# Performance work log

Hardware: AMD Instinct MI355X
Metric: run time of the kernel (lower is better)

Reference implementation:

```python
import jax, jax.numpy as jnp
import numpy as np

E = 1024   # embd_size
H = 16     # heads_num
DH = E // H
DFF = 4 * E
B, T = 2, 2048


def layer_norm(x, g, b, eps=1e-5):
    mu = jnp.mean(x, axis=-1, keepdims=True)
    var = jnp.var(x, axis=-1, keepdims=True)
    return (x - mu) * jax.lax.rsqrt(var + eps) * g + b


def setup_inputs() -> dict:
    key = jax.random.key(0)
    ks = jax.random.split(key, 12)
    s = 0.02
    return {
        "x": jax.random.normal(ks[0], (B, T, E), dtype=jnp.float32),
        "Wq": jax.random.normal(ks[1], (E, E), dtype=jnp.float32) * s,
        "Wk": jax.random.normal(ks[2], (E, E), dtype=jnp.float32) * s,
        "Wv": jax.random.normal(ks[3], (E, E), dtype=jnp.float32) * s,
        "Wo": jax.random.normal(ks[4], (E, E), dtype=jnp.float32) * s,
        "bo": jnp.zeros((E,), dtype=jnp.float32),
        "W1": jax.random.normal(ks[5], (E, DFF), dtype=jnp.float32) * s,
        "b1": jnp.zeros((DFF,), dtype=jnp.float32),
        "W2": jax.random.normal(ks[6], (DFF, E), dtype=jnp.float32) * s,
        "b2": jnp.zeros((E,), dtype=jnp.float32),
        "g1": jnp.ones((E,), dtype=jnp.float32),
        "be1": jnp.zeros((E,), dtype=jnp.float32),
        "g2": jnp.ones((E,), dtype=jnp.float32),
        "be2": jnp.zeros((E,), dtype=jnp.float32),
    }


def reference(x, Wq, Wk, Wv, Wo, bo, W1, b1, W2, b2, g1, be1, g2, be2):
    Bx, Tx, C = x.shape
    # --- self-attention sublayer ---
    h = layer_norm(x, g1, be1)
    # per-head projections; heads concatenated along output dim == stacked weights
    q = (h @ Wq).reshape(Bx, Tx, H, DH)  # [B,T,H,Dh]
    k = (h @ Wk).reshape(Bx, Tx, H, DH)
    v = (h @ Wv).reshape(Bx, Tx, H, DH)
    # NOTE: original scales by full embd_size**-0.5 (C = x.shape[-1]), not head_size
    scale = C ** (-0.5)
    scores = jnp.einsum("bqhd,bkhd->bhqk", q, k) * scale  # [B,H,T,T]
    mask = jnp.tril(jnp.ones((Tx, Tx), dtype=bool))
    scores = jnp.where(mask, scores, -jnp.inf)
    attn = jax.nn.softmax(scores, axis=-1)
    o = jnp.einsum("bhqk,bkhd->bqhd", attn, v).reshape(Bx, Tx, C)
    sa = o @ Wo + bo
    x = x + sa
    # --- feed-forward sublayer ---
    h2 = layer_norm(x, g2, be2)
    ff = jax.nn.relu(h2 @ W1 + b1) @ W2 + b2
    return x + ff
```

## Files before the change

### kernel.cpp

```cpp
#include <hip/hip_runtime.h>
#include <hip/hip_bf16.h>
#include <math.h>

#define Bn 2
#define Tn 2048
#define En 1024
#define Hn 16
#define DFFn 4096
#define Mn (Bn*Tn)
#define QKVLD 3072

typedef __hip_bfloat16 bf16;
typedef unsigned short u16;
typedef unsigned int u32;
typedef __attribute__((ext_vector_type(8))) short short8;
typedef __attribute__((ext_vector_type(4))) float f32x4;

typedef __attribute__((address_space(1))) const void cg_void;
typedef __attribute__((address_space(3))) void lds_void;

#define QSC 0.0450842200278f

#define HBAR() asm volatile("s_waitcnt lgkmcnt(0)\n\ts_barrier" ::: "memory")

__device__ __forceinline__ u16 f2bf(float f) {
    bf16 h = __float2bfloat16(f);
    u16 u; __builtin_memcpy(&u, &h, 2); return u;
}
__device__ __forceinline__ float bf2f(u16 u) {
    u32 x = ((u32)u) << 16; float f; __builtin_memcpy(&f, &x, 4); return f;
}

__global__ __launch_bounds__(256)
void transpose_w4(const float* __restrict__ s0, const float* __restrict__ s1,
                  const float* __restrict__ s2, const float* __restrict__ s3,
                  u16* __restrict__ d0, u16* __restrict__ d1,
                  u16* __restrict__ d2, u16* __restrict__ d3) {
    const float* src = (blockIdx.z == 0) ? s0 : (blockIdx.z == 1) ? s1
                     : (blockIdx.z == 2) ? s2 : s3;
    u16* dst = (blockIdx.z == 0) ? d0 : (blockIdx.z == 1) ? d1
             : (blockIdx.z == 2) ? d2 : d3;
    __shared__ float t[64][65];
    const int r0 = blockIdx.y * 64, c0 = blockIdx.x * 64;
    const int tr = threadIdx.x >> 6, tc = threadIdx.x & 63;
#pragma unroll
    for (int i = 0; i < 16; i++)
        t[tr + i * 4][tc] = src[(size_t)(r0 + tr + i * 4) * 1024 + c0 + tc];
    __syncthreads();
#pragma unroll
    for (int i = 0; i < 16; i++)
        dst[(size_t)(c0 + tr + i * 4) * 1024 + r0 + tc] = f2bf(t[tc][tr + i * 4]);
}

__global__ __launch_bounds__(256)
void transpose_w(const float* __restrict__ src, u16* __restrict__ dst,
                 int R, int C) {
    __shared__ float t[64][65];
    const int r0 = blockIdx.y * 64, c0 = blockIdx.x * 64;
    const int tr = threadIdx.x >> 6, tc = threadIdx.x & 63;
#pragma unroll
    for (int i = 0; i < 16; i++)
        t[tr + i * 4][tc] = src[(size_t)(r0 + tr + i * 4) * C + c0 + tc];
    __syncthreads();
#pragma unroll
    for (int i = 0; i < 16; i++)
        dst[(size_t)(c0 + tr + i * 4) * R + r0 + tc] = f2bf(t[tc][tr + i * 4]);
}

__global__ __launch_bounds__(256)
void vcopy_t(const u16* __restrict__ QKV, u16* __restrict__ Vg) {
    const int bh = blockIdx.z;
    const int t0 = blockIdx.y * 64;
    __shared__ u16 t[64][65];
    const int tr = threadIdx.x >> 6, tc = threadIdx.x & 63;
    const u16* src = QKV + (size_t)(bh >> 4) * 2048 * QKVLD + 2048 + (bh & 15) * 64;
#pragma unroll
    for (int i = 0; i < 16; i++)
        t[tr + i * 4][tc] = src[(size_t)(t0 + tr + i * 4) * QKVLD + tc];
    __syncthreads();
    u16* dst = Vg + (size_t)bh * 64 * 2048;
#pragma unroll
    for (int i = 0; i < 16; i++)
        dst[(size_t)(tr + i * 4) * 2048 + t0 + tc] = t[tc][tr + i * 4];
}

template<typename AT>
__global__ __launch_bounds__(256)
void ln_kernel(const AT* __restrict__ x, const float* __restrict__ g,
               const float* __restrict__ b, u16* __restrict__ out) {
    const int row = blockIdx.x;
    const int tid = threadIdx.x;
    const AT* xp = x + (size_t)row * En;
    float v[4];
    float s = 0.f, sq = 0.f;
#pragma unroll
    for (int i = 0; i < 4; i++) {
        if constexpr (sizeof(AT) == 2) v[i] = bf2f(xp[tid + i * 256]);
        else                           v[i] = (float)xp[tid + i * 256];
        s += v[i];
        sq += v[i] * v[i];
    }
    __shared__ float rs[256], rq[256];
    rs[tid] = s; rq[tid] = sq;
    __syncthreads();
    for (int st = 128; st > 0; st >>= 1) {
        if (tid < st) { rs[tid] += rs[tid + st]; rq[tid] += rq[tid + st]; }
        __syncthreads();
    }
    const float mu  = rs[0] * (1.0f / En);
    const float var = rq[0] * (1.0f / En) - mu * mu;
    const float inv = rsqrtf(var + 1e-5f);
#pragma unroll
    for (int i = 0; i < 4; i++) {
        const int c = tid + i * 256;
        out[(size_t)row * En + c] = f2bf((v[i] - mu) * inv * g[c] + b[c]);
    }
}

__global__ __launch_bounds__(256)
void ff2_init(const u16* __restrict__ X1, const float* __restrict__ b2,
              float* __restrict__ out) {
    const int row = blockIdx.x;
    const int c = threadIdx.x * 4;
    ushort4 a = *(const ushort4*)&X1[(size_t)row * En + c];
    float4 bb = *(const float4*)&b2[c];
    float4 o;
    o.x = bf2f(a.x) + bb.x;
    o.y = bf2f(a.y) + bb.y;
    o.z = bf2f(a.z) + bb.z;
    o.w = bf2f(a.w) + bb.w;
    *(float4*)&out[(size_t)row * En + c] = o;
}

template<int HAS_BIAS, int RELU, int SPLITC>
__global__ __launch_bounds__(512, 2)
void gemm256(const u16* __restrict__ A, int ldA,
             const u16* __restrict__ Wt, int ldW,
             const float* __restrict__ bias,
             u16* __restrict__ Cout, u16* __restrict__ Cout2,
             int ldC, int Kd) {
    __shared__ __align__(16) u16 As[2][256 * 64];
    __shared__ __align__(16) u16 Bs[2][256 * 64];
    const int tid  = threadIdx.x;
    const int lane = tid & 63, wv = tid >> 6;
    const int quad = lane >> 4, l16 = lane & 15;
    const int wr = wv >> 2, wc = wv & 3;
    const int lr8 = lane >> 3;
    const int gcg = (lane & 7) ^ lr8;

    const int m0 = blockIdx.y * 256, n0 = blockIdx.x * 256;

    f32x4 acc[8][4] = {};

    auto stage = [&](int buf, int kt) {
#pragma unroll
        for (int i = 0; i < 4; i++) {
            const int rbase = wv * 32 + i * 8;
            __builtin_amdgcn_global_load_lds(
                (cg_void*)(const void*)&A[(size_t)(m0 + rbase + lr8) * ldA + kt + gcg * 8],
                (lds_void*)(void*)&As[buf][rbase * 64], 16, 0, 0);
        }
#pragma unroll
        for (int i = 0; i < 4; i++) {
            const int rbase = wv * 32 + i * 8;
            __builtin_amdgcn_global_load_lds(
                (cg_void*)(const void*)&Wt[(size_t)(n0 + rbase + lr8) * ldW + kt + gcg * 8],
                (lds_void*)(void*)&Bs[buf][rbase * 64], 16, 0, 0);
        }
    };
    auto compute = [&](int buf) {
        const int swz = l16 & 7;
#pragma unroll
        for (int ks = 0; ks < 2; ks++) {
            short8 a[8], b[4];
#pragma unroll
            for (int mf = 0; mf < 8; mf++)
                a[mf] = *(const short8*)&As[buf][(wr * 128 + mf * 16 + l16) * 64 +
                         (((ks * 4 + quad) ^ swz) * 8)];
#pragma unroll
            for (int nf = 0; nf < 4; nf++)
                b[nf] = *(const short8*)&Bs[buf][(wc * 64 + nf * 16 + l16) * 64 +
                         (((ks * 4 + quad) ^ swz) * 8)];
#pragma unroll
            for (int mf = 0; mf < 8; mf++)
#pragma unroll
                for (int nf = 0; nf < 4; nf++)
                    acc[mf][nf] = __builtin_amdgcn_mfma_f32_16x16x32_bf16(
                        a[mf], b[nf], acc[mf][nf], 0, 0, 0);
        }
    };

    stage(0, 0);
    asm volatile("s_waitcnt vmcnt(0)" ::: "memory");
    __builtin_amdgcn_s_barrier();
    const int NT = Kd >> 6;
    for (int t = 0; t < NT; ++t) {
        const int cur = t & 1;
        if (t + 1 < NT) stage(cur ^ 1, (t + 1) * 64);
        compute(cur);
        asm volatile("s_waitcnt vmcnt(0) lgkmcnt(0)" ::: "memory");
        __builtin_amdgcn_s_barrier();
    }

#pragma unroll
    for (int mf = 0; mf < 8; mf++) {
#pragma unroll
        for (int r = 0; r < 4; r++) {
            const int gm = m0 + wr * 128 + mf * 16 + quad * 4 + r;
#pragma unroll
            for (int nf = 0; nf < 4; nf++) {
                const int gn = n0 + wc * 64 + nf * 16 + l16;
                const int cn = SPLITC ? (gn & 2047) : gn;
                float c = acc[mf][nf][r];
                if (HAS_BIAS) c += bias[gn];
                if (RELU) c = fmaxf(c, 0.f);
                u16* Cp = (SPLITC && gn >= 2048) ? Cout2 : Cout;
                Cp[(size_t)gm * ldC + cn] = f2bf(c);
            }
        }
    }
}

template<int TM, int HAS_BIAS, int RELU, int RES, int OUT_F32, int SCQ,
         int SPLITC, int SPLITA, int ATOM = 0, int XSWZ = 0, int PIPE = 0>
__global__ __launch_bounds__(256)
void gemm_bt(const u16* __restrict__ A, const u16* __restrict__ A2, int ldA,
             const u16* __restrict__ Wt, int ldW,
             const float* __restrict__ bias, const void* __restrict__ res,
             void* __restrict__ Cout, void* __restrict__ Cout2,
             int ldC, int Kd) {
    constexpr int IF = TM / 32;
    constexpr int LD = TM / 64 + 2;
    constexpr int RB = PIPE ? 4 : 1;
    __shared__ __align__(16) u16 As[RB][TM * 32];
    __shared__ __align__(16) u16 Bs[RB][128 * 32];
    const int tid  = threadIdx.x;
    const int lane = tid & 63, wv = tid >> 6;
    const int quad = lane >> 4, l16 = lane & 15;

    int bx = blockIdx.x, by = blockIdx.y, bz = blockIdx.z;
    if (XSWZ) {
        const int GX = gridDim.x, GY = gridDim.y;
        const int L = (bz * GY + by) * GX + bx;
        const int xcd = L & 7, slot = L >> 3;
        const int p = slot / GX;
        bx = slot - p * GX;
        const int yz = p * 8 + xcd;
        by = yz & (GY - 1);
        bz = yz >> __builtin_ctz(GY);
    }

    const int m0 = by * TM, n0 = bx * 128;
    const int rw = (wv >> 1) * (TM / 2), cw = (wv & 1) * 64;
    const int lr  = lane >> 2;
    const int gsw = ((lane & 3) ^ ((lane >> 3) & 3)) * 8;
    const int psw = (quad ^ ((l16 >> 1) & 3)) * 8;

    f32x4 acc[IF][4] = {};

    auto stage = [&](int buf, int kt) {
        const u16* Ap = (SPLITA && kt >= 2048) ? A2 : A;
        const int  kk = SPLITA ? (kt & 2047) : kt;
#pragma unroll
        for (int t = 0; t < TM / 64; t++) {
            const int row = wv * (TM / 4) + t * 16;
            __builtin_amdgcn_global_load_lds(
                (cg_void*)(const void*)&Ap[(size_t)(m0 + row + lr) * ldA + kk + gsw],
                (lds_void*)(void*)&As[buf][row * 32], 16, 0, 0);
        }
#pragma unroll
        for (int t = 0; t < 2; t++) {
            const int row = wv * 32 + t * 16;
            __builtin_amdgcn_global_load_lds(
                (cg_void*)(const void*)&Wt[(size_t)(n0 + row + lr) * ldW + kt + gsw],
                (lds_void*)(void*)&Bs[buf][row * 32], 16, 0, 0);
        }
    };
    auto compute = [&](int buf) {
        short8 af[IF], bfr[4];
#pragma unroll
        for (int i = 0; i < IF; i++)
            af[i] = *(const short8*)&As[buf][(rw + i * 16 + l16) * 32 + psw];
#pragma unroll
        for (int j = 0; j < 4; j++)
            bfr[j] = *(const short8*)&Bs[buf][(cw + j * 16 + l16) * 32 + psw];
#pragma unroll
        for (int i = 0; i < IF; i++)
#pragma unroll
            for (int j = 0; j < 4; j++)
                acc[i][j] = __builtin_amdgcn_mfma_f32_16x16x32_bf16(
                    af[i], bfr[j], acc[i][j], 0, 0, 0);
    };

    const int kbase = ATOM ? bz * Kd : 0;

    if constexpr (PIPE == 0) {
        for (int kt = kbase; kt < kbase + Kd; kt += 32) {
            __syncthreads();
            stage(0, kt);
            __syncthreads();
            compute(0);
        }
    } else {
        const int NI = Kd >> 5;
        stage(0, kbase);
        stage(1, kbase + 32);
        stage(2, kbase + 64);
        int bc = 0, bs = 3;
        for (int it = 0; it < NI; ++it) {
            if (it + 3 < NI) {
                stage(bs, kbase + (it + 3) * 32);
                if (++bs == RB) bs = 0;
            }
            const int rem = (NI - 1 - it) < 3 ? (NI - 1 - it) : 3;
            if (rem == 3) {
                if constexpr (LD == 4) asm volatile("s_waitcnt vmcnt(12)" ::: "memory");
                else                   asm volatile("s_waitcnt vmcnt(9)"  ::: "memory");
            } else if (rem == 2) {
                if constexpr (LD == 4) asm volatile("s_waitcnt vmcnt(8)"  ::: "memory");
                else                   asm volatile("s_waitcnt vmcnt(6)"  ::: "memory");
            } else if (rem == 1) {
                if constexpr (LD == 4) asm volatile("s_waitcnt vmcnt(4)"  ::: "memory");
                else                   asm volatile("s_waitcnt vmcnt(3)"  ::: "memory");
            } else {
                asm volatile("s_waitcnt vmcnt(0)" ::: "memory");
            }
            __builtin_amdgcn_s_barrier();
            compute(bc);
            if (++bc == RB) bc = 0;
            asm volatile("s_waitcnt lgkmcnt(0)" ::: "memory");
            __builtin_amdgcn_s_barrier();
        }
    }

    const float qscale = (SCQ && n0 < 1024) ? QSC : 1.0f;
    void* Cp = (SPLITC && n0 >= 2048) ? Cout2 : Cout;
#pragma unroll
    for (int i = 0; i < IF; i++) {
#pragma unroll
        for (int r = 0; r < 4; r++) {
            const int gm = m0 + rw + i * 16 + quad * 4 + r;
#pragma unroll
            for (int j = 0; j < 4; j++) {
                const int gn = n0 + cw + j * 16 + l16;
                const int cn = SPLITC ? (gn & 2047) : gn;
                float c = acc[i][j][r];
                if (HAS_BIAS) c += bias[gn];
                if (RELU) c = fmaxf(c, 0.f);
                if (RES == 1) c += ((const float*)res)[(size_t)gm * ldC + cn];
                if (RES == 2) c += bf2f(((const u16*)res)[(size_t)gm * ldC + cn]);
                if (SCQ) c *= qscale;
                if (ATOM) {
                    atomicAdd(&((float*)Cp)[(size_t)gm * ldC + cn], c);
                } else if (OUT_F32) {
                    ((float*)Cp)[(size_t)gm * ldC + cn] = c;
                } else {
                    ((u16*)Cp)[(size_t)gm * ldC + cn] = f2bf(c);
                }
            }
        }
    }
}

__global__ __launch_bounds__(256)
void flash_pass1(const u16* __restrict__ QKV, const u16* __restrict__ Vg,
                 u16* __restrict__ Op0, u16* __restrict__ Op1qkv,
                 float* __restrict__ stats) {
    const int pr = blockIdx.x >> 1, half = blockIdx.x & 1;
    const int hh = blockIdx.y, bb = blockIdx.z;
    const int tid  = threadIdx.x;
    const int lane = tid & 63, wv = tid >> 6;
    const int quad = lane >> 4, l16 = lane & 15;

    __shared__ __align__(16) u16 Ks[2][64 * 64];
    __shared__ __align__(16) u16 Vt[2][64 * 64];
    __shared__ __align__(16) u16 Ps[4][16 * 64];

    const size_t rowbase = (size_t)(bb * Tn) * QKVLD;
    const u16* Vgh = Vg + (size_t)(bb * Hn + hh) * 64 * 2048;

    const int sr = tid >> 2;
    const int p0 = (tid & 3) | ((sr & 1) << 2);
    const int p1 = p0 ^ 4;
    const int g0 = p0 ^ (sr & 7), g1 = p1 ^ (sr & 7);
    const int lsw = l16 & 7;

    uint4 kA, kB, vA, vB;
    auto prefetch = [&](int kt) {
        const size_t kb = rowbase + (size_t)(kt * 64 + sr) * QKVLD + 1024 + hh * 64;
        kA = *(const uint4*)&QKV[kb + g0 * 8];
        kB = *(const uint4*)&QKV[kb + g1 * 8];
        const size_t vb = (size_t)sr * 2048 + kt * 64;
        vA = *(const uint4*)&Vgh[vb + g0 * 8];
        vB = *(const uint4*)&Vgh[vb + g1 * 8];
    };
    auto writebuf = [&](int buf) {
        *(uint4*)&Ks[buf][sr * 64 + p0 * 8] = kA;
        *(uint4*)&Ks[buf][sr * 64 + p1 * 8] = kB;
        *(uint4*)&Vt[buf][sr * 64 + p0 * 8] = vA;
        *(uint4*)&Vt[buf][sr * 64 + p1 * 8] = vB;
    };

    for (int qsel = 0; qsel < 2; qsel++) {
        const int qt = qsel ? (31 - pr) : pr;
        const int nk = (qt >= half) ? ((qt - half) >> 1) + 1 : 0;
        const int qrow = qt * 64 + wv * 16 + l16;
        const int grow = bb * Tn + qrow;

        f32x4 ot[4] = {};
        float m2 = -INFINITY, lrow = 0.f;

        HBAR();
        if (nk > 0) {
            const u16* qp = QKV + rowbase + (size_t)qrow * QKVLD + hh * 64;
            short8 qf[2];
            qf[0] = *(const short8*)&qp[quad * 8];
            qf[1] = *(const short8*)&qp[32 + quad * 8];

            prefetch(half);
            writebuf(0);
            if (nk > 1) prefetch(half + 2);
            HBAR();

            const bool hasdiag = ((qt ^ half) & 1) == 0;
            for (int f = 0; f < nk; f++) {
                const int cur = f & 1;

                f32x4 st[4] = {};
#pragma unroll
                for (int ks = 0; ks < 2; ks++)
#pragma unroll
                    for (int i = 0; i < 4; i++) {
                        short8 kf = *(const short8*)&Ks[cur][(i * 16 + l16) * 64 +
                                     (((ks * 4 + quad) ^ lsw) * 8)];
                        st[i] = __builtin_amdgcn_mfma_f32_16x16x32_bf16(
                            kf, qf[ks], st[i], 0, 0, 0);
                    }

                float tmax = -INFINITY;
                if (hasdiag && f == nk - 1) {
                    const int qloc = wv * 16 + l16;
#pragma unroll
                    for (int i = 0; i < 4; i++)
#pragma unroll
                        for (int r = 0; r < 4; r++) {
                            float s = st[i][r];
                            if (i * 16 + quad * 4 + r > qloc) s = -INFINITY;
                            st[i][r] = s;
                            tmax = fmaxf(tmax, s);
                        }
                } else {
#pragma unroll
                    for (int i = 0; i < 4; i++)
#pragma unroll
                        for (int r = 0; r < 4; r++)
                            tmax = fmaxf(tmax, st[i][r]);
                }
                tmax = fmaxf(tmax, __shfl_xor(tmax, 16));
                tmax = fmaxf(tmax, __shfl_xor(tmax, 32));

                const float mnew = fmaxf(m2, tmax);
                const float alpha = exp2f(m2 - mnew);
                m2 = mnew;
                float psum = 0.f;
#pragma unroll
                for (int i = 0; i < 4; i++)
#pragma unroll
                    for (int r = 0; r < 4; r++) {
                        const float e = exp2f(st[i][r] - mnew);
                        st[i][r] = e;
                        psum += e;
                    }
                psum += __shfl_xor(psum, 16);
                psum += __shfl_xor(psum, 32);
                lrow = lrow * alpha + psum;
#pragma unroll
                for (int i = 0; i < 4; i++) ot[i] *= alpha;

#pragma unroll
                for (int i = 0; i < 4; i++) {
                    uint2 w;
                    w.x = (u32)f2bf(st[i][0]) | ((u32)f2bf(st[i][1]) << 16);
                    w.y = (u32)f2bf(st[i][2]) | ((u32)f2bf(st[i][3]) << 16);
                    const int g = (i * 2 + (quad >> 1)) ^ lsw;
                    *(uint2*)&Ps[wv][l16 * 64 + g * 8 + (quad & 1) * 4] = w;
                }
                asm volatile("s_waitcnt lgkmcnt(0)" ::: "memory");

#pragma unroll
                for (int ks = 0; ks < 2; ks++) {
                    short8 pf = *(const short8*)&Ps[wv][l16 * 64 +
                                 (((ks * 4 + quad) ^ lsw) * 8)];
#pragma unroll
                    for (int i = 0; i < 4; i++) {
                        short8 vf = *(const short8*)&Vt[cur][(i * 16 + l16) * 64 +
                                     (((ks * 4 + quad) ^ lsw) * 8)];
                        ot[i] = __builtin_amdgcn_mfma_f32_16x16x32_bf16(
                            vf, pf, ot[i], 0, 0, 0);
                    }
                }

                if (f + 1 < nk) {
                    writebuf(cur ^ 1);
                    if (f + 2 < nk) prefetch(half + 2 * (f + 2));
                    HBAR();
                }
            }
        }

        u16* op = (half == 0) ? (Op0 + (size_t)grow * 1024 + hh * 64)
                              : (Op1qkv + (size_t)grow * QKVLD + 2048 + hh * 64);
#pragma unroll
        for (int i = 0; i < 4; i++) {
            ushort4 o4;
            o4.x = f2bf(ot[i][0]); o4.y = f2bf(ot[i][1]);
            o4.z = f2bf(ot[i][2]); o4.w = f2bf(ot[i][3]);
            *(ushort4*)&op[i * 16 + quad * 4] = o4;
        }
        if (quad == 0) {
            stats[((size_t)(half * 2 + 0) * 4096 + grow) * 16 + hh] = m2;
            stats[((size_t)(half * 2 + 1) * 4096 + grow) * 16 + hh] = lrow;
        }
    }
}

__global__ __launch_bounds__(256)
void flash_merge(u16* __restrict__ QKV, const u16* __restrict__ Op0,
                 const float* __restrict__ stats) {
    const int row = blockIdx.x;
    const int tid = threadIdx.x;
    const int col = tid * 4;
    const int hh = col >> 6;
    const float m0 = stats[((size_t)0 * 4096 + row) * 16 + hh];
    const float l0 = stats[((size_t)1 * 4096 + row) * 16 + hh];
    const float m1 = stats[((size_t)2 * 4096 + row) * 16 + hh];
    const float l1 = stats[((size_t)3 * 4096 + row) * 16 + hh];
    const float m  = fmaxf(m0, m1);
    const float w0 = exp2f(m0 - m), w1 = exp2f(m1 - m);
    const float inv = 1.0f / (w0 * l0 + w1 * l1);
    ushort4 a = *(const ushort4*)&Op0[(size_t)row * 1024 + col];
    ushort4 b = *(const ushort4*)&QKV[(size_t)row * QKVLD + 2048 + col];
    ushort4 o;
    o.x = f2bf((w0 * bf2f(a.x) + w1 * bf2f(b.x)) * inv);
    o.y = f2bf((w0 * bf2f(a.y) + w1 * bf2f(b.y)) * inv);
    o.z = f2bf((w0 * bf2f(a.z) + w1 * bf2f(b.z)) * inv);
    o.w = f2bf((w0 * bf2f(a.w) + w1 * bf2f(b.w)) * inv);
    *(ushort4*)&QKV[(size_t)row * QKVLD + col] = o;
}

extern "C" void kernel_launch(void* const* d_in, const int* in_sizes, int n_in,
                              void* d_out, int out_size, void* d_ws, size_t ws_size,
                              hipStream_t stream) {
    const float* x   = (const float*)d_in[0];
    const float* Wq  = (const float*)d_in[1];
    const float* Wk  = (const float*)d_in[2];
    const float* Wv  = (const float*)d_in[3];
    const float* Wo  = (const float*)d_in[4];
    const float* bo  = (const float*)d_in[5];
    const float* W1  = (const float*)d_in[6];
    const float* b1  = (const float*)d_in[7];
    const float* W2  = (const float*)d_in[8];
    const float* b2  = (const float*)d_in[9];
    const float* g1  = (const float*)d_in[10];
    const float* be1 = (const float*)d_in[11];
    const float* g2  = (const float*)d_in[12];
    const float* be2 = (const float*)d_in[13];

    char* wsb = (char*)d_ws;
    u16*   QKV = (u16*)wsb;
    u16*   F1a = (u16*)wsb;
    u16*   W2T = (u16*)(wsb + 16u * 1024 * 1024);
    u16*   Op0 = (u16*)(wsb + 24u * 1024 * 1024);
    u16*   X1b = Op0;
    u16*   Vg  = (u16*)(wsb + 32u * 1024 * 1024);
    u16*   F1b = Vg;
    u16*   h     = (u16*)d_out;
    u16*   WT    = (u16*)((char*)d_out + 8u * 1024 * 1024);
    u16*   WqkvT = WT;
    u16*   WoT   = WT + 3u * 1024 * 1024;
    float* stats = (float*)WT;
    u16*   W1T   = WT;

    transpose_w4<<<dim3(16, 16, 4), 256, 0, stream>>>(
        Wq, Wk, Wv, Wo,
        WqkvT, WqkvT + 1024u * 1024, WqkvT + 2048u * 1024, WoT);

    ln_kernel<float><<<Mn, 256, 0, stream>>>(x, g1, be1, h);

    gemm_bt<128, 0, 0, 0, 0, 1, 0, 0, 0, 1, 0><<<dim3(24, 32), 256, 0, stream>>>(
        h, nullptr, En, WqkvT, En, nullptr, nullptr, QKV, nullptr, QKVLD, En);

    vcopy_t<<<dim3(1, 32, 32), 256, 0, stream>>>(QKV, Vg);

    flash_pass1<<<dim3(32, Hn, Bn), 256, 0, stream>>>(QKV, Vg, Op0, QKV, stats);

    flash_merge<<<Mn, 256, 0, stream>>>(QKV, Op0, stats);

    gemm_bt<64, 1, 0, 1, 0, 0, 0, 0, 0, 1, 0><<<dim3(8, 64), 256, 0, stream>>>(
        QKV, nullptr, QKVLD, WoT, En, bo, x, X1b, nullptr, En, En);

    transpose_w<<<dim3(64, 16), 256, 0, stream>>>(W1, W1T, 1024, 4096);
    transpose_w<<<dim3(16, 64), 256, 0, stream>>>(W2, W2T, 4096, 1024);

    ln_kernel<u16><<<Mn, 256, 0, stream>>>(X1b, g2, be2, h);

    gemm256<1, 1, 1><<<dim3(16, 16), 512, 0, stream>>>(
        h, En, W1T, En, b1, F1a, F1b, 2048, En);

    ff2_init<<<Mn, 256, 0, stream>>>(X1b, b2, (float*)d_out);

    gemm_bt<128, 0, 0, 0, 1, 0, 0, 1, 1, 1, 1><<<dim3(8, 32, 2), 256, 0, stream>>>(
        F1a, F1b, 2048, W2T, DFFn, nullptr, nullptr, (float*)d_out, nullptr,
        En, 2048);
}
```

Before: 373.1 us.

## Generalize 256-row GEMM kernel and use it for QKV and FF2 projections

Templatizes the 256x256 double-buffered GEMM over tile width, Q scaling, split-K atomic accumulation, and split A inputs. The QKV projection and the FF2 split-K GEMM now run on this larger-tile 512-thread kernel in place of the 128-tile gemm_bt. The 4-stage pipelined path in gemm_bt is removed. The aim is more data reuse per block and fewer LDS round trips per MFMA, at the cost of fewer blocks (192 and 256) in flight on a large-CU GPU.

```diff
diff --git a/kernel.cpp b/kernel.cpp
--- a/kernel.cpp
+++ b/kernel.cpp
@@ -132,39 +132,46 @@
     *(float4*)&out[(size_t)row * En + c] = o;
 }
 
-template<int HAS_BIAS, int RELU, int SPLITC>
+template<int TN, int HAS_BIAS, int RELU, int SPLITC, int SCQ, int ATOM,
+         int SPLITA>
 __global__ __launch_bounds__(512, 2)
-void gemm256(const u16* __restrict__ A, int ldA,
+void gemm256(const u16* __restrict__ A, const u16* __restrict__ A2, int ldA,
              const u16* __restrict__ Wt, int ldW,
              const float* __restrict__ bias,
              u16* __restrict__ Cout, u16* __restrict__ Cout2,
-             int ldC, int Kd) {
+             float* __restrict__ outF, int ldC, int Kd) {
+    constexpr int WGN = (TN == 256) ? 4 : 2;
+    constexpr int MF  = (256 / (8 / WGN)) / 16;
+    constexpr int NF  = (TN / WGN) / 16;
     __shared__ __align__(16) u16 As[2][256 * 64];
-    __shared__ __align__(16) u16 Bs[2][256 * 64];
+    __shared__ __align__(16) u16 Bs[2][TN * 64];
     const int tid  = threadIdx.x;
     const int lane = tid & 63, wv = tid >> 6;
     const int quad = lane >> 4, l16 = lane & 15;
-    const int wr = wv >> 2, wc = wv & 3;
+    const int wr = wv / WGN, wc = wv % WGN;
     const int lr8 = lane >> 3;
     const int gcg = (lane & 7) ^ lr8;
 
-    const int m0 = blockIdx.y * 256, n0 = blockIdx.x * 256;
-
-    f32x4 acc[8][4] = {};
+    const int m0 = blockIdx.y * 256, n0 = blockIdx.x * TN;
+    const int bz = ATOM ? blockIdx.z : 0;
+    const u16* Ap = (SPLITA && bz) ? A2 : A;
+    const int kbase = ATOM ? bz * Kd : 0;
+
+    f32x4 acc[MF][NF] = {};
 
     auto stage = [&](int buf, int kt) {
 #pragma unroll
         for (int i = 0; i < 4; i++) {
             const int rbase = wv * 32 + i * 8;
             __builtin_amdgcn_global_load_lds(
-                (cg_void*)(const void*)&A[(size_t)(m0 + rbase + lr8) * ldA + kt + gcg * 8],
+                (cg_void*)(const void*)&Ap[(size_t)(m0 + rbase + lr8) * ldA + kt + gcg * 8],
                 (lds_void*)(void*)&As[buf][rbase * 64], 16, 0, 0);
         }
 #pragma unroll
-        for (int i = 0; i < 4; i++) {
-            const int rbase = wv * 32 + i * 8;
+        for (int i = 0; i < TN / 64; i++) {
+            const int rbase = wv * (TN / 8) + i * 8;
             __builtin_amdgcn_global_load_lds(
-                (cg_void*)(const void*)&Wt[(size_t)(n0 + rbase + lr8) * ldW + kt + gcg * 8],
+                (cg_void*)(const void*)&Wt[(size_t)(n0 + rbase + lr8) * ldW + kbase + kt + gcg * 8],
                 (lds_void*)(void*)&Bs[buf][rbase * 64], 16, 0, 0);
         }
     };
@@ -172,19 +179,19 @@
         const int swz = l16 & 7;
 #pragma unroll
         for (int ks = 0; ks < 2; ks++) {
-            short8 a[8], b[4];
-#pragma unroll
-            for (int mf = 0; mf < 8; mf++)
-                a[mf] = *(const short8*)&As[buf][(wr * 128 + mf * 16 + l16) * 64 +
+            short8 a[MF], b[NF];
+#pragma unroll
+            for (int mf = 0; mf < MF; mf++)
+                a[mf] = *(const short8*)&As[buf][(wr * (MF * 16) + mf * 16 + l16) * 64 +
                          (((ks * 4 + quad) ^ swz) * 8)];
 #pragma unroll
-            for (int nf = 0; nf < 4; nf++)
+            for (int nf = 0; nf < NF; nf++)
                 b[nf] = *(const short8*)&Bs[buf][(wc * 64 + nf * 16 + l16) * 64 +
                          (((ks * 4 + quad) ^ swz) * 8)];
 #pragma unroll
-            for (int mf = 0; mf < 8; mf++)
-#pragma unroll
-                for (int nf = 0; nf < 4; nf++)
+            for (int mf = 0; mf < MF; mf++)
+#pragma unroll
+                for (int nf = 0; nf < NF; nf++)
                     acc[mf][nf] = __builtin_amdgcn_mfma_f32_16x16x32_bf16(
                         a[mf], b[nf], acc[mf][nf], 0, 0, 0);
         }
@@ -202,20 +209,26 @@
         __builtin_amdgcn_s_barrier();
     }
 
-#pragma unroll
-    for (int mf = 0; mf < 8; mf++) {
+    const float qscale = (SCQ && n0 < 1024) ? QSC : 1.0f;
+#pragma unroll
+    for (int mf = 0; mf < MF; mf++) {
 #pragma unroll
         for (int r = 0; r < 4; r++) {
-            const int gm = m0 + wr * 128 + mf * 16 + quad * 4 + r;
-#pragma unroll
-            for (int nf = 0; nf < 4; nf++) {
+            const int gm = m0 + wr * (MF * 16) + mf * 16 + quad * 4 + r;
+#pragma unroll
+            for (int nf = 0; nf < NF; nf++) {
                 const int gn = n0 + wc * 64 + nf * 16 + l16;
                 const int cn = SPLITC ? (gn & 2047) : gn;
                 float c = acc[mf][nf][r];
                 if (HAS_BIAS) c += bias[gn];
                 if (RELU) c = fmaxf(c, 0.f);
-                u16* Cp = (SPLITC && gn >= 2048) ? Cout2 : Cout;
-                Cp[(size_t)gm * ldC + cn] = f2bf(c);
+                if (SCQ) c *= qscale;
+                if (ATOM) {
+                    atomicAdd(&outF[(size_t)gm * ldC + gn], c);
+                } else {
+                    u16* Cp = (SPLITC && gn >= 2048) ? Cout2 : Cout;
+                    Cp[(size_t)gm * ldC + cn] = f2bf(c);
+                }
             }
         }
     }
@@ -230,8 +243,7 @@
              void* __restrict__ Cout, void* __restrict__ Cout2,
              int ldC, int Kd) {
     constexpr int IF = TM / 32;
-    constexpr int LD = TM / 64 + 2;
-    constexpr int RB = PIPE ? 4 : 1;
+    constexpr int RB = 1;
     __shared__ __align__(16) u16 As[RB][TM * 32];
     __shared__ __align__(16) u16 Bs[RB][128 * 32];
     const int tid  = threadIdx.x;
@@ -293,44 +305,11 @@
     };
 
     const int kbase = ATOM ? bz * Kd : 0;
-
-    if constexpr (PIPE == 0) {
-        for (int kt = kbase; kt < kbase + Kd; kt += 32) {
-            __syncthreads();
-            stage(0, kt);
-            __syncthreads();
-            compute(0);
-        }
-    } else {
-        const int NI = Kd >> 5;
-        stage(0, kbase);
-        stage(1, kbase + 32);
-        stage(2, kbase + 64);
-        int bc = 0, bs = 3;
-        for (int it = 0; it < NI; ++it) {
-            if (it + 3 < NI) {
-                stage(bs, kbase + (it + 3) * 32);
-                if (++bs == RB) bs = 0;
-            }
-            const int rem = (NI - 1 - it) < 3 ? (NI - 1 - it) : 3;
-            if (rem == 3) {
-                if constexpr (LD == 4) asm volatile("s_waitcnt vmcnt(12)" ::: "memory");
-                else                   asm volatile("s_waitcnt vmcnt(9)"  ::: "memory");
-            } else if (rem == 2) {
-                if constexpr (LD == 4) asm volatile("s_waitcnt vmcnt(8)"  ::: "memory");
-                else                   asm volatile("s_waitcnt vmcnt(6)"  ::: "memory");
-            } else if (rem == 1) {
-                if constexpr (LD == 4) asm volatile("s_waitcnt vmcnt(4)"  ::: "memory");
-                else                   asm volatile("s_waitcnt vmcnt(3)"  ::: "memory");
-            } else {
-                asm volatile("s_waitcnt vmcnt(0)" ::: "memory");
-            }
-            __builtin_amdgcn_s_barrier();
-            compute(bc);
-            if (++bc == RB) bc = 0;
-            asm volatile("s_waitcnt lgkmcnt(0)" ::: "memory");
-            __builtin_amdgcn_s_barrier();
-        }
+    for (int kt = kbase; kt < kbase + Kd; kt += 32) {
+        __syncthreads();
+        stage(0, kt);
+        __syncthreads();
+        compute(0);
     }
 
     const float qscale = (SCQ && n0 < 1024) ? QSC : 1.0f;
@@ -587,8 +566,8 @@
 
     ln_kernel<float><<<Mn, 256, 0, stream>>>(x, g1, be1, h);
 
-    gemm_bt<128, 0, 0, 0, 0, 1, 0, 0, 0, 1, 0><<<dim3(24, 32), 256, 0, stream>>>(
-        h, nullptr, En, WqkvT, En, nullptr, nullptr, QKV, nullptr, QKVLD, En);
+    gemm256<256, 0, 0, 0, 1, 0, 0><<<dim3(12, 16), 512, 0, stream>>>(
+        h, nullptr, En, WqkvT, En, nullptr, QKV, nullptr, nullptr, QKVLD, En);
 
     vcopy_t<<<dim3(1, 32, 32), 256, 0, stream>>>(QKV, Vg);
 
@@ -604,12 +583,12 @@
 
     ln_kernel<u16><<<Mn, 256, 0, stream>>>(X1b, g2, be2, h);
 
-    gemm256<1, 1, 1><<<dim3(16, 16), 512, 0, stream>>>(
-        h, En, W1T, En, b1, F1a, F1b, 2048, En);
+    gemm256<256, 1, 1, 1, 0, 0, 0><<<dim3(16, 16), 512, 0, stream>>>(
+        h, nullptr, En, W1T, En, b1, F1a, F1b, nullptr, 2048, En);
 
     ff2_init<<<Mn, 256, 0, stream>>>(X1b, b2, (float*)d_out);
 
-    gemm_bt<128, 0, 0, 0, 1, 0, 0, 1, 1, 1, 1><<<dim3(8, 32, 2), 256, 0, stream>>>(
-        F1a, F1b, 2048, W2T, DFFn, nullptr, nullptr, (float*)d_out, nullptr,
-        En, 2048);
-}
+    gemm256<128, 0, 0, 0, 0, 1, 1><<<dim3(8, 16, 2), 512, 0, stream>>>(
+        F1a, F1b, 2048, W2T, DFFn, nullptr, nullptr, nullptr,
+        (float*)d_out, En, 2048);
+}
```

Result: no change. 375.4 us (+0.6%).
